# Kernel tuning notes

Hardware: AMD Instinct MI355X
Metric: run time of the kernel (lower is better)

## Reference

```python
import jax, jax.numpy as jnp
import numpy as np

B, N_C, Y_DIM = 8, 2048, 8
GRID_RES = 128
GRID_MIN, GRID_MAX = -1.0, 1.0
SIGMA0 = 0.1


def _make_grid_points():
    x = jnp.linspace(GRID_MIN, GRID_MAX, GRID_RES, dtype=jnp.float32)
    y = jnp.linspace(GRID_MIN, GRID_MAX, GRID_RES, dtype=jnp.float32)
    gy, gx = jnp.meshgrid(y, x, indexing='ij')
    return jnp.stack([gx, gy], axis=-1).reshape(1, -1, 2)  # (1, R*R, 2)


def setup_inputs() -> dict:
    key = jax.random.key(0)
    k1, k2 = jax.random.split(key)
    x_c = jax.random.uniform(k1, (B, N_C, 2), dtype=jnp.float32, minval=GRID_MIN, maxval=GRID_MAX)
    y_c = jax.random.normal(k2, (B, N_C, Y_DIM), dtype=jnp.float32)
    grid_points = _make_grid_points()
    sigma = jnp.asarray(SIGMA0, dtype=jnp.float32)
    return {"x_c": x_c, "y_c": y_c, "grid_points": grid_points, "sigma": sigma}


def reference(x_c, y_c, grid_points, sigma):
    g = grid_points[0]                                    # (M, 2)
    xn = jnp.sum(x_c * x_c, axis=-1)                      # (B, N)
    gn = jnp.sum(g * g, axis=-1)                          # (M,)
    cross = jnp.einsum('bnd,md->bnm', x_c, g)             # (B, N, M)
    d2 = xn[:, :, None] + gn[None, None, :] - 2.0 * cross # (B, N, M)
    weights = jnp.exp(-0.5 * d2 / (sigma * sigma))        # (B, N, M)
    density = jnp.sum(weights, axis=1)                    # (B, M)
    signal = jnp.einsum('bny,bnm->bym', y_c, weights)     # (B, Y, M)
    normalized = signal / (density[:, None, :] + 1e-5)
    out = jnp.concatenate([density[:, None, :], normalized], axis=1)  # (B, 1+Y, M)
    return out.reshape(x_c.shape[0], -1, GRID_RES, GRID_RES)
```

## Files before the change

### kernel.cpp

```cpp
#include <hip/hip_runtime.h>


typedef float  f32x4 __attribute__((ext_vector_type(4)));
typedef __fp16 half8  __attribute__((ext_vector_type(8)));
typedef __fp16 half2t __attribute__((ext_vector_type(2)));

constexpr int B_  = 8;
constexpr int NC  = 2048;
constexpr int M_  = 128 * 128;
constexpr int BLK = 512;
constexpr int KW  = 256;
constexpr int LDHY = NC + 8;

constexpr int OFF_SXT = 0;
constexpr int OFF_SYT = OFF_SXT + NC * 4;
constexpr int OFF_SYS = OFF_SYT + NC * 4;
constexpr int OFF_SG  = OFF_SYS + 8 * LDHY * 2;
constexpr int SLOT_F  = 2 * 9 * 256;
constexpr int POOL_B  = 4 * SLOT_F * 4;

__global__ __launch_bounds__(BLK, 2) void rbf_sep(
    const float* __restrict__ x_c,
    const float* __restrict__ y_c,
    const float* __restrict__ gp,
    const float* __restrict__ sigma_p,
    float* __restrict__ out)
{
    __shared__ __align__(16) char pool[POOL_B];
    float*  sxt = (float*)(pool + OFF_SXT);
    float*  syt = (float*)(pool + OFF_SYT);
    __fp16* sys = (__fp16*)(pool + OFF_SYS);
    float*  sg  = (float*)(pool + OFF_SG);

    const int tid  = (int)threadIdx.x;
    const int lane = tid & 63;
    const int w    = tid >> 6;
    const int q    = lane >> 4;
    const int cl   = lane & 15;

    const int bid = blockIdx.x;
    const int b   = bid >> 5;
    const int myg = (bid >> 3) & 3;
    const int mxg = bid & 7;
    const int my0 = myg * 32;
    const int mx0 = mxg * 16;

    const float sigma = sigma_p[0];
    const float s = __builtin_sqrtf(0.72134752044448170f) / sigma;

    if (tid < 32)      sg[tid] = s * gp[(my0 + tid) * 256 + 1];
    else if (tid < 48) sg[tid] = s * gp[(mx0 + (tid - 32)) * 2];

    const float2* xb = (const float2*)x_c + (size_t)b * NC;
    const float4* yb = (const float4*)y_c + (size_t)b * NC * 2;
    for (int it = tid; it < NC; it += BLK) {
        const float2 v = xb[it];
        sxt[it] = s * v.x;
        syt[it] = s * v.y;
        const float4 y0 = yb[(size_t)it * 2];
        const float4 y1 = yb[(size_t)it * 2 + 1];
        __fp16* yw = sys + it;
        yw[0 * LDHY] = (__fp16)y0.x;
        yw[1 * LDHY] = (__fp16)y0.y;
        yw[2 * LDHY] = (__fp16)y0.z;
        yw[3 * LDHY] = (__fp16)y0.w;
        yw[4 * LDHY] = (__fp16)y1.x;
        yw[5 * LDHY] = (__fp16)y1.y;
        yw[6 * LDHY] = (__fp16)y1.z;
        yw[7 * LDHY] = (__fp16)y1.w;
    }
    __syncthreads();

    const float sgy0 = sg[cl];
    const float sgy1 = sg[16 + cl];
    const float sgxr = sg[32 + cl];

    f32x4 acc[2][9];
#pragma unroll
    for (int t = 0; t < 2; ++t)
#pragma unroll
        for (int c = 0; c < 9; ++c) acc[t][c] = (f32x4)0.0f;

    const int kbase = w * KW;
#pragma unroll 2
    for (int ks = 0; ks < KW / 32; ++ks) {
        const int kq = kbase + ks * 32 + q * 8;

        const f32x4 ya0 = *(const f32x4*)(syt + kq);
        const f32x4 ya1 = *(const f32x4*)(syt + kq + 4);
        const f32x4 xa0 = *(const f32x4*)(sxt + kq);
        const f32x4 xa1 = *(const f32x4*)(sxt + kq + 4);

        const f32x4 y0e0 = ya0 - sgy0, y0e1 = ya1 - sgy0;
        const f32x4 y0m0 = y0e0 * y0e0, y0m1 = y0e1 * y0e1;
        const half2t p00 = __builtin_amdgcn_cvt_pkrtz(
            __builtin_amdgcn_exp2f(-y0m0.x), __builtin_amdgcn_exp2f(-y0m0.y));
        const half2t p01 = __builtin_amdgcn_cvt_pkrtz(
            __builtin_amdgcn_exp2f(-y0m0.z), __builtin_amdgcn_exp2f(-y0m0.w));
        const half2t p02 = __builtin_amdgcn_cvt_pkrtz(
            __builtin_amdgcn_exp2f(-y0m1.x), __builtin_amdgcn_exp2f(-y0m1.y));
        const half2t p03 = __builtin_amdgcn_cvt_pkrtz(
            __builtin_amdgcn_exp2f(-y0m1.z), __builtin_amdgcn_exp2f(-y0m1.w));
        const half8 af0 = (half8){p00.x, p00.y, p01.x, p01.y, p02.x, p02.y, p03.x, p03.y};

        const f32x4 y1e0 = ya0 - sgy1, y1e1 = ya1 - sgy1;
        const f32x4 y1m0 = y1e0 * y1e0, y1m1 = y1e1 * y1e1;
        const half2t p10 = __builtin_amdgcn_cvt_pkrtz(
            __builtin_amdgcn_exp2f(-y1m0.x), __builtin_amdgcn_exp2f(-y1m0.y));
        const half2t p11 = __builtin_amdgcn_cvt_pkrtz(
            __builtin_amdgcn_exp2f(-y1m0.z), __builtin_amdgcn_exp2f(-y1m0.w));
        const half2t p12 = __builtin_amdgcn_cvt_pkrtz(
            __builtin_amdgcn_exp2f(-y1m1.x), __builtin_amdgcn_exp2f(-y1m1.y));
        const half2t p13 = __builtin_amdgcn_cvt_pkrtz(
            __builtin_amdgcn_exp2f(-y1m1.z), __builtin_amdgcn_exp2f(-y1m1.w));
        const half8 af1 = (half8){p10.x, p10.y, p11.x, p11.y, p12.x, p12.y, p13.x, p13.y};

        const f32x4 xe0 = xa0 - sgxr, xe1 = xa1 - sgxr;
        const f32x4 xm0 = xe0 * xe0,   xm1 = xe1 * xe1;
        const half2t b0 = __builtin_amdgcn_cvt_pkrtz(
            __builtin_amdgcn_exp2f(-xm0.x), __builtin_amdgcn_exp2f(-xm0.y));
        const half2t b1 = __builtin_amdgcn_cvt_pkrtz(
            __builtin_amdgcn_exp2f(-xm0.z), __builtin_amdgcn_exp2f(-xm0.w));
        const half2t b2 = __builtin_amdgcn_cvt_pkrtz(
            __builtin_amdgcn_exp2f(-xm1.x), __builtin_amdgcn_exp2f(-xm1.y));
        const half2t b3 = __builtin_amdgcn_cvt_pkrtz(
            __builtin_amdgcn_exp2f(-xm1.z), __builtin_amdgcn_exp2f(-xm1.w));
        const half8 bx = (half8){b0.x, b0.y, b1.x, b1.y, b2.x, b2.y, b3.x, b3.y};

        acc[0][0] = __builtin_amdgcn_mfma_f32_16x16x32_f16(af0, bx, acc[0][0], 0, 0, 0);
        acc[1][0] = __builtin_amdgcn_mfma_f32_16x16x32_f16(af1, bx, acc[1][0], 0, 0, 0);
        const __fp16* yp = sys + kq;
#pragma unroll
        for (int c = 0; c < 8; ++c) {
            const half8 yf  = *(const half8*)(yp + c * LDHY);
            const half8 bxy = bx * yf;
            acc[0][c + 1] = __builtin_amdgcn_mfma_f32_16x16x32_f16(af0, bxy, acc[0][c + 1], 0, 0, 0);
            acc[1][c + 1] = __builtin_amdgcn_mfma_f32_16x16x32_f16(af1, bxy, acc[1][c + 1], 0, 0, 0);
        }
    }

    __syncthreads();
    float* slots = (float*)pool;
    if (w >= 4) {
        float* rb = slots + (w - 4) * SLOT_F;
#pragma unroll
        for (int t = 0; t < 2; ++t)
#pragma unroll
            for (int c = 0; c < 9; ++c)
#pragma unroll
                for (int r = 0; r < 4; ++r)
                    rb[t * 2304 + c * 256 + (q * 4 + r) * 16 + cl] = acc[t][c][r];
    }
    __syncthreads();
    if (w < 4) {
        float* rb = slots + w * SLOT_F;
#pragma unroll
        for (int t = 0; t < 2; ++t)
#pragma unroll
            for (int c = 0; c < 9; ++c)
#pragma unroll
                for (int r = 0; r < 4; ++r) {
                    const int idx = t * 2304 + c * 256 + (q * 4 + r) * 16 + cl;
                    rb[idx] = rb[idx] + acc[t][c][r];
                }
    }
    __syncthreads();

    {
        float* ob = out + (size_t)b * 9 * M_;
        const int t  = tid >> 8;
        const int my = (tid >> 4) & 15;
        const int mx = tid & 15;
        const size_t mo = (size_t)(my0 + t * 16 + my) * 128 + mx0 + mx;
        float v[9];
#pragma unroll
        for (int c = 0; c < 9; ++c) {
            const int idx = t * 2304 + c * 256 + my * 16 + mx;
            v[c] = (slots[idx] + slots[SLOT_F + idx]) +
                   (slots[2 * SLOT_F + idx] + slots[3 * SLOT_F + idx]);
        }
        const float inv = __builtin_amdgcn_rcpf(v[0] + 1e-5f);
        ob[mo] = v[0];
#pragma unroll
        for (int c = 1; c < 9; ++c)
            ob[(size_t)c * M_ + mo] = v[c] * inv;
    }
}

extern "C" void kernel_launch(void* const* d_in, const int* in_sizes, int n_in,
                              void* d_out, int out_size, void* d_ws, size_t ws_size,
                              hipStream_t stream) {
    const float* x_c   = (const float*)d_in[0];
    const float* y_c   = (const float*)d_in[1];
    const float* gp    = (const float*)d_in[2];
    const float* sigma = (const float*)d_in[3];
    float* out = (float*)d_out;

    dim3 grid(B_ * 32);
    dim3 block(BLK);
    rbf_sep<<<grid, block, 0, stream>>>(x_c, y_c, gp, sigma, out);
}
```

Measured before the change: 16.80 us.

## Pre-transpose y_c to fp16 in a separate kernel and read it from global

Adds a small pre-pass kernel that converts y_c to fp16 and transposes it into channel-major layout in workspace. The main kernel no longer stages y into LDS; each lane loads its half8 y fragments straight from global/L2 inside the k loop. This shrinks the LDS prologue and the LDS footprint. In exchange it adds a second launch and puts global load latency inside the MFMA loop.

```diff
diff --git a/kernel.cpp b/kernel.cpp
--- a/kernel.cpp
+++ b/kernel.cpp
@@ -10,27 +10,48 @@
 constexpr int M_  = 128 * 128;
 constexpr int BLK = 512;
 constexpr int KW  = 256;
-constexpr int LDHY = NC + 8;
 
 constexpr int OFF_SXT = 0;
 constexpr int OFF_SYT = OFF_SXT + NC * 4;
-constexpr int OFF_SYS = OFF_SYT + NC * 4;
-constexpr int OFF_SG  = OFF_SYS + 8 * LDHY * 2;
+constexpr int OFF_SG  = OFF_SYT + NC * 4;
 constexpr int SLOT_F  = 2 * 9 * 256;
 constexpr int POOL_B  = 4 * SLOT_F * 4;
 
+__global__ __launch_bounds__(256) void transpose_y(
+    const float* __restrict__ y_c, __fp16* __restrict__ yt)
+{
+    __shared__ __fp16 ly[8][264];
+    const int t  = (int)threadIdx.x;
+    const int b  = blockIdx.x >> 3;
+    const int k0 = (blockIdx.x & 7) * 256;
+
+    const float4* yb = (const float4*)(y_c + ((size_t)b * NC + k0) * 8);
+    const float4 a  = yb[2 * t];
+    const float4 c4 = yb[2 * t + 1];
+    ly[0][t] = (__fp16)a.x;  ly[1][t] = (__fp16)a.y;
+    ly[2][t] = (__fp16)a.z;  ly[3][t] = (__fp16)a.w;
+    ly[4][t] = (__fp16)c4.x; ly[5][t] = (__fp16)c4.y;
+    ly[6][t] = (__fp16)c4.z; ly[7][t] = (__fp16)c4.w;
+    __syncthreads();
+
+    const int ch = t >> 5, kk = (t & 31) * 8;
+    half8 v;
+#pragma unroll
+    for (int j = 0; j < 8; ++j) v[j] = ly[ch][kk + j];
+    *(half8*)(yt + ((size_t)b * 8 + ch) * NC + k0 + kk) = v;
+}
+
 __global__ __launch_bounds__(BLK, 2) void rbf_sep(
     const float* __restrict__ x_c,
-    const float* __restrict__ y_c,
+    const __fp16* __restrict__ yt,
     const float* __restrict__ gp,
     const float* __restrict__ sigma_p,
     float* __restrict__ out)
 {
     __shared__ __align__(16) char pool[POOL_B];
-    float*  sxt = (float*)(pool + OFF_SXT);
-    float*  syt = (float*)(pool + OFF_SYT);
-    __fp16* sys = (__fp16*)(pool + OFF_SYS);
-    float*  sg  = (float*)(pool + OFF_SG);
+    float* sxt = (float*)(pool + OFF_SXT);
+    float* syt = (float*)(pool + OFF_SYT);
+    float* sg  = (float*)(pool + OFF_SG);
 
     const int tid  = (int)threadIdx.x;
     const int lane = tid & 63;
@@ -52,28 +73,18 @@
     else if (tid < 48) sg[tid] = s * gp[(mx0 + (tid - 32)) * 2];
 
     const float2* xb = (const float2*)x_c + (size_t)b * NC;
-    const float4* yb = (const float4*)y_c + (size_t)b * NC * 2;
     for (int it = tid; it < NC; it += BLK) {
         const float2 v = xb[it];
         sxt[it] = s * v.x;
         syt[it] = s * v.y;
-        const float4 y0 = yb[(size_t)it * 2];
-        const float4 y1 = yb[(size_t)it * 2 + 1];
-        __fp16* yw = sys + it;
-        yw[0 * LDHY] = (__fp16)y0.x;
-        yw[1 * LDHY] = (__fp16)y0.y;
-        yw[2 * LDHY] = (__fp16)y0.z;
-        yw[3 * LDHY] = (__fp16)y0.w;
-        yw[4 * LDHY] = (__fp16)y1.x;
-        yw[5 * LDHY] = (__fp16)y1.y;
-        yw[6 * LDHY] = (__fp16)y1.z;
-        yw[7 * LDHY] = (__fp16)y1.w;
     }
     __syncthreads();
 
     const float sgy0 = sg[cl];
     const float sgy1 = sg[16 + cl];
     const float sgxr = sg[32 + cl];
+
+    const __fp16* ytb = yt + (size_t)b * 8 * NC;
 
     f32x4 acc[2][9];
 #pragma unroll
@@ -85,6 +96,11 @@
 #pragma unroll 2
     for (int ks = 0; ks < KW / 32; ++ks) {
         const int kq = kbase + ks * 32 + q * 8;
+
+        half8 yf[8];
+#pragma unroll
+        for (int c = 0; c < 8; ++c)
+            yf[c] = *(const half8*)(ytb + c * NC + kq);
 
         const f32x4 ya0 = *(const f32x4*)(syt + kq);
         const f32x4 ya1 = *(const f32x4*)(syt + kq + 4);
@@ -129,11 +145,9 @@
 
         acc[0][0] = __builtin_amdgcn_mfma_f32_16x16x32_f16(af0, bx, acc[0][0], 0, 0, 0);
         acc[1][0] = __builtin_amdgcn_mfma_f32_16x16x32_f16(af1, bx, acc[1][0], 0, 0, 0);
-        const __fp16* yp = sys + kq;
 #pragma unroll
         for (int c = 0; c < 8; ++c) {
-            const half8 yf  = *(const half8*)(yp + c * LDHY);
-            const half8 bxy = bx * yf;
+            const half8 bxy = bx * yf[c];
             acc[0][c + 1] = __builtin_amdgcn_mfma_f32_16x16x32_f16(af0, bxy, acc[0][c + 1], 0, 0, 0);
             acc[1][c + 1] = __builtin_amdgcn_mfma_f32_16x16x32_f16(af1, bxy, acc[1][c + 1], 0, 0, 0);
         }
@@ -194,9 +208,11 @@
     const float* y_c   = (const float*)d_in[1];
     const float* gp    = (const float*)d_in[2];
     const float* sigma = (const float*)d_in[3];
-    float* out = (float*)d_out;
+    float* out  = (float*)d_out;
+    __fp16* yt  = (__fp16*)d_ws;
+
+    transpose_y<<<dim3(B_ * 8), dim3(256), 0, stream>>>(y_c, yt);
 
     dim3 grid(B_ * 32);
-    dim3 block(BLK);
-    rbf_sep<<<grid, block, 0, stream>>>(x_c, y_c, gp, sigma, out);
+    rbf_sep<<<grid, dim3(BLK), 0, stream>>>(x_c, yt, gp, sigma, out);
 }
```

New measurement: 28.85 us. 1.72x slower.

## Double-buffer LDS operand loads in MFMA loop and vectorize reduction stores

Applied to the files above, without the earlier changes.

Software-pipelines the main K loop with two register buffers, so the LDS reads for step k+1, including all eight y fragments, are issued before step k's exp and MFMA work. It also changes the cross-wave reduction scratch to a lane-major layout, so each accumulator is stored and read as one 16-byte vector instead of four scalars, and the final gather index is remapped to match. The cost is higher register pressure from holding two full operand sets, which could cause spills or reduce occupancy under the launch bounds.

```diff
diff --git a/kernel.cpp b/kernel.cpp
--- a/kernel.cpp
+++ b/kernel.cpp
@@ -16,7 +16,7 @@
 constexpr int OFF_SYT = OFF_SXT + NC * 4;
 constexpr int OFF_SYS = OFF_SYT + NC * 4;
 constexpr int OFF_SG  = OFF_SYS + 8 * LDHY * 2;
-constexpr int SLOT_F  = 2 * 9 * 256;
+constexpr int SLOT_F  = 2 * 9 * 64 * 4;
 constexpr int POOL_B  = 4 * SLOT_F * 4;
 
 __global__ __launch_bounds__(BLK, 2) void rbf_sep(
@@ -81,63 +81,82 @@
 #pragma unroll
         for (int c = 0; c < 9; ++c) acc[t][c] = (f32x4)0.0f;
 
-    const int kbase = w * KW;
-#pragma unroll 2
-    for (int ks = 0; ks < KW / 32; ++ks) {
-        const int kq = kbase + ks * 32 + q * 8;
-
-        const f32x4 ya0 = *(const f32x4*)(syt + kq);
-        const f32x4 ya1 = *(const f32x4*)(syt + kq + 4);
-        const f32x4 xa0 = *(const f32x4*)(sxt + kq);
-        const f32x4 xa1 = *(const f32x4*)(sxt + kq + 4);
-
-        const f32x4 y0e0 = ya0 - sgy0, y0e1 = ya1 - sgy0;
-        const f32x4 y0m0 = y0e0 * y0e0, y0m1 = y0e1 * y0e1;
-        const half2t p00 = __builtin_amdgcn_cvt_pkrtz(
-            __builtin_amdgcn_exp2f(-y0m0.x), __builtin_amdgcn_exp2f(-y0m0.y));
-        const half2t p01 = __builtin_amdgcn_cvt_pkrtz(
-            __builtin_amdgcn_exp2f(-y0m0.z), __builtin_amdgcn_exp2f(-y0m0.w));
-        const half2t p02 = __builtin_amdgcn_cvt_pkrtz(
-            __builtin_amdgcn_exp2f(-y0m1.x), __builtin_amdgcn_exp2f(-y0m1.y));
-        const half2t p03 = __builtin_amdgcn_cvt_pkrtz(
-            __builtin_amdgcn_exp2f(-y0m1.z), __builtin_amdgcn_exp2f(-y0m1.w));
-        const half8 af0 = (half8){p00.x, p00.y, p01.x, p01.y, p02.x, p02.y, p03.x, p03.y};
-
-        const f32x4 y1e0 = ya0 - sgy1, y1e1 = ya1 - sgy1;
-        const f32x4 y1m0 = y1e0 * y1e0, y1m1 = y1e1 * y1e1;
-        const half2t p10 = __builtin_amdgcn_cvt_pkrtz(
-            __builtin_amdgcn_exp2f(-y1m0.x), __builtin_amdgcn_exp2f(-y1m0.y));
-        const half2t p11 = __builtin_amdgcn_cvt_pkrtz(
-            __builtin_amdgcn_exp2f(-y1m0.z), __builtin_amdgcn_exp2f(-y1m0.w));
-        const half2t p12 = __builtin_amdgcn_cvt_pkrtz(
-            __builtin_amdgcn_exp2f(-y1m1.x), __builtin_amdgcn_exp2f(-y1m1.y));
-        const half2t p13 = __builtin_amdgcn_cvt_pkrtz(
-            __builtin_amdgcn_exp2f(-y1m1.z), __builtin_amdgcn_exp2f(-y1m1.w));
-        const half8 af1 = (half8){p10.x, p10.y, p11.x, p11.y, p12.x, p12.y, p13.x, p13.y};
-
-        const f32x4 xe0 = xa0 - sgxr, xe1 = xa1 - sgxr;
-        const f32x4 xm0 = xe0 * xe0,   xm1 = xe1 * xe1;
-        const half2t b0 = __builtin_amdgcn_cvt_pkrtz(
-            __builtin_amdgcn_exp2f(-xm0.x), __builtin_amdgcn_exp2f(-xm0.y));
-        const half2t b1 = __builtin_amdgcn_cvt_pkrtz(
-            __builtin_amdgcn_exp2f(-xm0.z), __builtin_amdgcn_exp2f(-xm0.w));
-        const half2t b2 = __builtin_amdgcn_cvt_pkrtz(
-            __builtin_amdgcn_exp2f(-xm1.x), __builtin_amdgcn_exp2f(-xm1.y));
-        const half2t b3 = __builtin_amdgcn_cvt_pkrtz(
-            __builtin_amdgcn_exp2f(-xm1.z), __builtin_amdgcn_exp2f(-xm1.w));
-        const half8 bx = (half8){b0.x, b0.y, b1.x, b1.y, b2.x, b2.y, b3.x, b3.y};
-
-        acc[0][0] = __builtin_amdgcn_mfma_f32_16x16x32_f16(af0, bx, acc[0][0], 0, 0, 0);
-        acc[1][0] = __builtin_amdgcn_mfma_f32_16x16x32_f16(af1, bx, acc[1][0], 0, 0, 0);
-        const __fp16* yp = sys + kq;
-#pragma unroll
-        for (int c = 0; c < 8; ++c) {
-            const half8 yf  = *(const half8*)(yp + c * LDHY);
-            const half8 bxy = bx * yf;
-            acc[0][c + 1] = __builtin_amdgcn_mfma_f32_16x16x32_f16(af0, bxy, acc[0][c + 1], 0, 0, 0);
-            acc[1][c + 1] = __builtin_amdgcn_mfma_f32_16x16x32_f16(af1, bxy, acc[1][c + 1], 0, 0, 0);
+    const int kbase = w * KW + q * 8;
+
+    f32x4 Aya0, Aya1, Axa0, Axa1; half8 Ayf[8];
+    f32x4 Bya0, Bya1, Bxa0, Bxa1; half8 Byf[8];
+
+#define LOADSTEP(ks, Y0, Y1, X0, X1, YF)                         \
+    {                                                            \
+        const int kq = kbase + (ks) * 32;                        \
+        Y0 = *(const f32x4*)(syt + kq);                          \
+        Y1 = *(const f32x4*)(syt + kq + 4);                      \
+        X0 = *(const f32x4*)(sxt + kq);                          \
+        X1 = *(const f32x4*)(sxt + kq + 4);                      \
+        _Pragma("unroll")                                        \
+        for (int c = 0; c < 8; ++c)                              \
+            YF[c] = *(const half8*)(sys + c * LDHY + kq);        \
+    }
+
+#define COMPUTE(Y0, Y1, X0, X1, YF)                                               \
+    {                                                                             \
+        const f32x4 y0e0 = Y0 - sgy0, y0e1 = Y1 - sgy0;                           \
+        const f32x4 y0m0 = y0e0 * y0e0, y0m1 = y0e1 * y0e1;                       \
+        const half2t p00 = __builtin_amdgcn_cvt_pkrtz(                            \
+            __builtin_amdgcn_exp2f(-y0m0.x), __builtin_amdgcn_exp2f(-y0m0.y));    \
+        const half2t p01 = __builtin_amdgcn_cvt_pkrtz(                            \
+            __builtin_amdgcn_exp2f(-y0m0.z), __builtin_amdgcn_exp2f(-y0m0.w));    \
+        const half2t p02 = __builtin_amdgcn_cvt_pkrtz(                            \
+            __builtin_amdgcn_exp2f(-y0m1.x), __builtin_amdgcn_exp2f(-y0m1.y));    \
+        const half2t p03 = __builtin_amdgcn_cvt_pkrtz(                            \
+            __builtin_amdgcn_exp2f(-y0m1.z), __builtin_amdgcn_exp2f(-y0m1.w));    \
+        const half8 af0 = (half8){p00.x, p00.y, p01.x, p01.y,                     \
+                                  p02.x, p02.y, p03.x, p03.y};                    \
+        const f32x4 y1e0 = Y0 - sgy1, y1e1 = Y1 - sgy1;                           \
+        const f32x4 y1m0 = y1e0 * y1e0, y1m1 = y1e1 * y1e1;                       \
+        const half2t p10 = __builtin_amdgcn_cvt_pkrtz(                            \
+            __builtin_amdgcn_exp2f(-y1m0.x), __builtin_amdgcn_exp2f(-y1m0.y));    \
+        const half2t p11 = __builtin_amdgcn_cvt_pkrtz(                            \
+            __builtin_amdgcn_exp2f(-y1m0.z), __builtin_amdgcn_exp2f(-y1m0.w));    \
+        const half2t p12 = __builtin_amdgcn_cvt_pkrtz(                            \
+            __builtin_amdgcn_exp2f(-y1m1.x), __builtin_amdgcn_exp2f(-y1m1.y));    \
+        const half2t p13 = __builtin_amdgcn_cvt_pkrtz(                            \
+            __builtin_amdgcn_exp2f(-y1m1.z), __builtin_amdgcn_exp2f(-y1m1.w));    \
+        const half8 af1 = (half8){p10.x, p10.y, p11.x, p11.y,                     \
+                                  p12.x, p12.y, p13.x, p13.y};                    \
+        const f32x4 xe0 = X0 - sgxr, xe1 = X1 - sgxr;                             \
+        const f32x4 xm0 = xe0 * xe0,  xm1 = xe1 * xe1;                            \
+        const half2t b0 = __builtin_amdgcn_cvt_pkrtz(                             \
+            __builtin_amdgcn_exp2f(-xm0.x), __builtin_amdgcn_exp2f(-xm0.y));      \
+        const half2t b1 = __builtin_amdgcn_cvt_pkrtz(                             \
+            __builtin_amdgcn_exp2f(-xm0.z), __builtin_amdgcn_exp2f(-xm0.w));      \
+        const half2t b2 = __builtin_amdgcn_cvt_pkrtz(                             \
+            __builtin_amdgcn_exp2f(-xm1.x), __builtin_amdgcn_exp2f(-xm1.y));      \
+        const half2t b3 = __builtin_amdgcn_cvt_pkrtz(                             \
+            __builtin_amdgcn_exp2f(-xm1.z), __builtin_amdgcn_exp2f(-xm1.w));      \
+        const half8 bx = (half8){b0.x, b0.y, b1.x, b1.y, b2.x, b2.y, b3.x, b3.y}; \
+        acc[0][0] = __builtin_amdgcn_mfma_f32_16x16x32_f16(af0, bx, acc[0][0], 0, 0, 0); \
+        acc[1][0] = __builtin_amdgcn_mfma_f32_16x16x32_f16(af1, bx, acc[1][0], 0, 0, 0); \
+        _Pragma("unroll")                                                         \
+        for (int c = 0; c < 8; ++c) {                                             \
+            const half8 bxy = bx * YF[c];                                         \
+            acc[0][c + 1] = __builtin_amdgcn_mfma_f32_16x16x32_f16(af0, bxy, acc[0][c + 1], 0, 0, 0); \
+            acc[1][c + 1] = __builtin_amdgcn_mfma_f32_16x16x32_f16(af1, bxy, acc[1][c + 1], 0, 0, 0); \
+        }                                                                         \
+    }
+
+    LOADSTEP(0, Aya0, Aya1, Axa0, Axa1, Ayf)
+#pragma unroll
+    for (int ks = 0; ks < 8; ks += 2) {
+        LOADSTEP(ks + 1, Bya0, Bya1, Bxa0, Bxa1, Byf)
+        COMPUTE(Aya0, Aya1, Axa0, Axa1, Ayf)
+        if (ks + 2 < 8) {
+            LOADSTEP(ks + 2, Aya0, Aya1, Axa0, Axa1, Ayf)
         }
-    }
+        COMPUTE(Bya0, Bya1, Bxa0, Bxa1, Byf)
+    }
+#undef LOADSTEP
+#undef COMPUTE
 
     __syncthreads();
     float* slots = (float*)pool;
@@ -147,9 +166,7 @@
         for (int t = 0; t < 2; ++t)
 #pragma unroll
             for (int c = 0; c < 9; ++c)
-#pragma unroll
-                for (int r = 0; r < 4; ++r)
-                    rb[t * 2304 + c * 256 + (q * 4 + r) * 16 + cl] = acc[t][c][r];
+                *(f32x4*)(rb + ((t * 9 + c) * 64 + lane) * 4) = acc[t][c];
     }
     __syncthreads();
     if (w < 4) {
@@ -157,12 +174,10 @@
 #pragma unroll
         for (int t = 0; t < 2; ++t)
 #pragma unroll
-            for (int c = 0; c < 9; ++c)
-#pragma unroll
-                for (int r = 0; r < 4; ++r) {
-                    const int idx = t * 2304 + c * 256 + (q * 4 + r) * 16 + cl;
-                    rb[idx] = rb[idx] + acc[t][c][r];
-                }
+            for (int c = 0; c < 9; ++c) {
+                float* p = rb + ((t * 9 + c) * 64 + lane) * 4;
+                *(f32x4*)p = *(const f32x4*)p + acc[t][c];
+            }
     }
     __syncthreads();
 
@@ -172,10 +187,11 @@
         const int my = (tid >> 4) & 15;
         const int mx = tid & 15;
         const size_t mo = (size_t)(my0 + t * 16 + my) * 128 + mx0 + mx;
+        const int eidx = ((my >> 2) * 16 + mx) * 4 + (my & 3);
         float v[9];
 #pragma unroll
         for (int c = 0; c < 9; ++c) {
-            const int idx = t * 2304 + c * 256 + my * 16 + mx;
+            const int idx = (t * 9 + c) * 256 + eidx;
             v[c] = (slots[idx] + slots[SLOT_F + idx]) +
                    (slots[2 * SLOT_F + idx] + slots[3 * SLOT_F + idx]);
         }
```

New measurement: 15.64 us (median of 2 runs). -7.0%, faster.
